# Kernel tuning notes

Hardware: AMD Instinct MI355X
Metric: run time of the kernel (lower is better)

The kernel has to match this reference:

```python
import jax, jax.numpy as jnp
import numpy as np

B, T, I = 64, 512, 512      # batch, timesteps, input feature dim
H1, H2 = 256, 128           # prenet hiddens
C = 1024                    # GRU channels
M = 80                      # mel bins
L = 2                       # residual GRU layers


def setup_inputs() -> dict:
    key = jax.random.key(0)
    ks = jax.random.split(key, 10)
    s = 0.02
    w = lambda k, shape: (jax.random.normal(k, shape, jnp.float32) * s)
    return {
        "inputs": jax.random.normal(ks[0], (B, T, I), jnp.float32),
        # prenet: Linear(M->H1) + ReLU, Linear(H1->H2) + ReLU (dropout off / eval)
        "pre_w0": w(ks[1], (H1, M)), "pre_b0": jnp.zeros((H1,), jnp.float32),
        "pre_w1": w(ks[2], (H2, H1)), "pre_b1": jnp.zeros((H2,), jnp.float32),
        # attention GRU: input I+H2 -> C (PyTorch gate layout [r|z|n])
        "attn_w_ih": w(ks[3], (3 * C, I + H2)), "attn_w_hh": w(ks[4], (3 * C, C)),
        "attn_b_ih": jnp.zeros((3 * C,), jnp.float32), "attn_b_hh": jnp.zeros((3 * C,), jnp.float32),
        # L residual GRUs: C -> C, stacked on leading axis
        "gru_w_ih": w(ks[5], (L, 3 * C, C)), "gru_w_hh": w(ks[6], (L, 3 * C, C)),
        "gru_b_ih": jnp.zeros((L, 3 * C), jnp.float32), "gru_b_hh": jnp.zeros((L, 3 * C), jnp.float32),
        # projection C -> M
        "proj_w": w(ks[7], (M, C)), "proj_b": jnp.zeros((M,), jnp.float32),
    }


def gru_cell(x, h, w_ih, w_hh, b_ih, b_hh):
    # PyTorch GRUCell math, gates ordered [r, z, n]
    gi = x @ w_ih.T + b_ih
    gh = h @ w_hh.T + b_hh
    i_r, i_z, i_n = jnp.split(gi, 3, axis=-1)
    h_r, h_z, h_n = jnp.split(gh, 3, axis=-1)
    r = jax.nn.sigmoid(i_r + h_r)
    z = jax.nn.sigmoid(i_z + h_z)
    n = jnp.tanh(i_n + r * h_n)
    return (1.0 - z) * n + z * h


def reference(inputs, pre_w0, pre_b0, pre_w1, pre_b1,
              attn_w_ih, attn_w_hh, attn_b_ih, attn_b_hh,
              gru_w_ih, gru_w_hh, gru_b_ih, gru_b_hh,
              proj_w, proj_b):
    bsz = inputs.shape[0]
    chan = attn_w_hh.shape[1]
    nlayers = gru_w_ih.shape[0]
    mel = proj_w.shape[0]

    def step(carry, feat):  # feat: [B, I]
        frame, attnh, hidd = carry  # [B,M], [B,C], [L,B,C]
        # prenet on previous frame (dropout disabled, eval-mode reference)
        p = jax.nn.relu(jax.nn.relu(frame @ pre_w0.T + pre_b0) @ pre_w1.T + pre_b1)
        attnh = gru_cell(jnp.concatenate([feat, p], axis=-1), attnh,
                         attn_w_ih, attn_w_hh, attn_b_ih, attn_b_hh)
        x = attnh
        new_hidd = []
        for l in range(nlayers):  # small fixed layer count
            h = gru_cell(x, hidd[l], gru_w_ih[l], gru_w_hh[l], gru_b_ih[l], gru_b_hh[l])
            x = x + h
            new_hidd.append(h)
        frame = x @ proj_w.T + proj_b
        return (frame, attnh, jnp.stack(new_hidd)), frame

    init = (jnp.zeros((bsz, mel), inputs.dtype),
            jnp.zeros((bsz, chan), inputs.dtype),
            jnp.zeros((nlayers, bsz, chan), inputs.dtype))
    _, frames = jax.lax.scan(step, init, jnp.swapaxes(inputs, 0, 1))  # [T,B,M]
    return jnp.swapaxes(frames, 0, 1)  # [B,T,M]
```

## Files before the change

### kernel.cpp

```cpp
#include <hip/hip_runtime.h>
#include <cstddef>


namespace {

constexpr int kB = 64, kT = 512, kI = 512, kH1 = 256, kH2 = 128, kC = 1024, kM = 80;

typedef __attribute__((ext_vector_type(8))) __bf16 bf16x8;
typedef __attribute__((ext_vector_type(4))) float f32x4;

__device__ __forceinline__ float sigm(float x) { return 1.0f / (1.0f + __expf(-x)); }
__device__ __forceinline__ float tanh_(float x) {
  float a = fabsf(x);
  float e = __expf(-2.0f * a);
  float r = (1.0f - e) / (1.0f + e);
  return copysignf(r, x);
}
__device__ __forceinline__ unsigned short f2bf(float x) {
  unsigned u = __builtin_bit_cast(unsigned, x);
  u += 0x7fffu + ((u >> 16) & 1u);
  return (unsigned short)(u >> 16);
}
__device__ __forceinline__ bf16x8 asbf(uint4 v) { return __builtin_bit_cast(bf16x8, v); }
__device__ __forceinline__ f32x4 mfma16(bf16x8 a, bf16x8 b, f32x4 c) {
  return __builtin_amdgcn_mfma_f32_16x16x32_bf16(a, b, c, 0, 0, 0);
}

__global__ __launch_bounds__(256) void k_build_frags(
    const float* __restrict__ srcA, int ldA,
    const float* __restrict__ srcB, int ldB,
    int row0, int K1, int nks, int nrt, unsigned short* __restrict__ dst) {
  int idx = blockIdx.x * 256 + threadIdx.x;
  int lane = idx & 63;
  int ks = (idx >> 6) % nks;
  int rt = idx / (64 * nks);
  if (rt >= nrt) return;
  int row = row0 + rt * 16 + (lane & 15);
  int kk = ks * 32 + ((lane >> 4) & 3) * 8;
  const float* s = (kk < K1) ? (srcA + (size_t)row * ldA + kk)
                             : (srcB + (size_t)row * ldB + (kk - K1));
  unsigned short* d = dst + ((size_t)(rt * nks + ks) * 64 + lane) * 8;
#pragma unroll
  for (int j = 0; j < 8; ++j) d[j] = f2bf(s[j]);
}

__global__ __launch_bounds__(256) void k_transpose(const float* __restrict__ src,
    int R, int Ccols, float* __restrict__ dst) {
  int i = blockIdx.x * 256 + threadIdx.x;
  if (i >= R * Ccols) return;
  int r = i / Ccols, c = i % Ccols;
  dst[c * R + r] = src[r * Ccols + c];
}

__global__ __launch_bounds__(256) void k_prenet(
    const float* __restrict__ inputs, int t,
    const float* __restrict__ pproj,
    const float* __restrict__ proj_b,
    const float* __restrict__ w0t, const float* __restrict__ b0,
    const float* __restrict__ w1t, const float* __restrict__ b1,
    unsigned short* __restrict__ xcat0_cur,
    float* __restrict__ out_frames) {
  int b = blockIdx.x, tid = threadIdx.x;
  __shared__ float sfr[kM];
  __shared__ float sh[kH1];
  __shared__ float sred[160];
  const float* feat = inputs + ((size_t)b * kT + t) * kI;
  unsigned short* dst = xcat0_cur + (size_t)b * 1664;
  float2 f2v = *(const float2*)(feat + tid * 2);
  dst[tid * 2] = f2bf(f2v.x);
  dst[tid * 2 + 1] = f2bf(f2v.y);
  if (t > 0) {
    if (tid < 160) {
      int m = tid >> 1, half = tid & 1;
      const float* pp = pproj + ((size_t)(half * 32) * kM + m) * kB + b;
      float s = 0.0f;
#pragma unroll 8
      for (int r = 0; r < 32; ++r) s += pp[(size_t)r * kM * kB];
      sred[tid] = s;
    }
    __syncthreads();
    if (tid < kM) {
      float f = proj_b[tid] + sred[tid * 2] + sred[tid * 2 + 1];
      sfr[tid] = f;
      out_frames[(size_t)b * kT * kM + (size_t)(t - 1) * kM + tid] = f;
    }
  } else {
    if (tid < kM) sfr[tid] = 0.0f;
  }
  __syncthreads();
  float acc = b0[tid];
#pragma unroll 8
  for (int m = 0; m < kM; ++m) acc = fmaf(w0t[m * kH1 + tid], sfr[m], acc);
  sh[tid] = fmaxf(acc, 0.0f);
  __syncthreads();
  if (tid < kH2) {
    float a = b1[tid];
#pragma unroll 8
    for (int k = 0; k < kH1; ++k) a = fmaf(w1t[k * kH2 + tid], sh[k], a);
    dst[512 + tid] = f2bf(fmaxf(a, 0.0f));
  }
}

template<int NKS, int NB, int BROW>
__global__ __launch_bounds__(512) void k_gru(
    const unsigned short* __restrict__ Ar, const unsigned short* __restrict__ Az,
    const unsigned short* __restrict__ An,
    const unsigned short* __restrict__ Bsrc,
    const float* __restrict__ h_old,
    const float* __restrict__ bih, const float* __restrict__ bhh,
    const float* __restrict__ xin_f32,
    float* __restrict__ h_new_f32,
    unsigned short* __restrict__ h_bf16, int hStride, int hOff,
    unsigned short* __restrict__ x_bf16, int xStride,
    float* __restrict__ xout_f32,
    const float* __restrict__ pw, float* __restrict__ pproj) {
  __shared__ float red[8 * 4 * 64 * 4];
  __shared__ float sx[16 * 16];
  int tid = threadIdx.x;
  int lane = tid & 63, w = tid >> 6, quad = lane >> 4;
  int xcd = blockIdx.x & 7, slot = blockIdx.x >> 3;
  int rt = xcd * 8 + (slot >> 2);
  int bt = slot & 3;
  int b = bt * 16 + (lane & 15);
  int s = (w * NKS) >> 3, e = ((w + 1) * NKS) >> 3;
  const uint4* Bq = (const uint4*)Bsrc + (size_t)b * BROW + quad;
  const uint4* Arq = (const uint4*)Ar + (size_t)rt * NKS * 64 + lane;
  const uint4* Azq = (const uint4*)Az + (size_t)rt * NKS * 64 + lane;
  const uint4* Anq = (const uint4*)An + (size_t)rt * NKS * 64 + lane;
  f32x4 aR = {0.f, 0.f, 0.f, 0.f}, aZ = aR, aNI = aR, aNH = aR;
  for (int ks = s; ks < e; ++ks) {
    bf16x8 bv = asbf(Bq[ks * 4]);
    aR = mfma16(asbf(Arq[ks * 64]), bv, aR);
    aZ = mfma16(asbf(Azq[ks * 64]), bv, aZ);
    if (ks < NB) aNI = mfma16(asbf(Anq[ks * 64]), bv, aNI);
    else         aNH = mfma16(asbf(Anq[ks * 64]), bv, aNH);
  }
  *(f32x4*)(red + ((w * 4 + 0) * 64 + lane) * 4) = aR;
  *(f32x4*)(red + ((w * 4 + 1) * 64 + lane) * 4) = aZ;
  *(f32x4*)(red + ((w * 4 + 2) * 64 + lane) * 4) = aNI;
  *(f32x4*)(red + ((w * 4 + 3) * 64 + lane) * 4) = aNH;
  __syncthreads();
  if (w < 4) {
    int q = lane >> 4, bb = lane & 15;
    float R = 0.f, Z = 0.f, NI = 0.f, NH = 0.f;
#pragma unroll
    for (int ww = 0; ww < 8; ++ww) {
      int base = (ww * 4 * 64 + w * 16 + bb) * 4 + q;
      R  += red[base];
      Z  += red[base + 64 * 4];
      NI += red[base + 2 * 64 * 4];
      NH += red[base + 3 * 64 * 4];
    }
    int c = rt * 16 + w * 4 + q;
    float r = sigm(R + bih[c] + bhh[c]);
    float z = sigm(Z + bih[kC + c] + bhh[kC + c]);
    float n = tanh_(NI + bih[2 * kC + c] + r * (NH + bhh[2 * kC + c]));
    float hold = h_old[c * kB + b];
    float hn = (1.0f - z) * n + z * hold;
    h_new_f32[c * kB + b] = hn;
    h_bf16[(size_t)b * hStride + hOff + c] = f2bf(hn);
    float xo = xin_f32 ? (xin_f32[c * kB + b] + hn) : hn;
    if (x_bf16) x_bf16[(size_t)b * xStride + c] = f2bf(xo);
    if (xout_f32) xout_f32[c * kB + b] = xo;
    if (pw) sx[(w * 4 + q) * 16 + bb] = xo;
  }
  if (pw) {
    __syncthreads();
    for (int idx = tid; idx < kM * 16; idx += 512) {
      int m = idx >> 4, bb = idx & 15;
      const float* wrow = pw + (size_t)m * kC + rt * 16;
      float a = 0.f;
#pragma unroll
      for (int c16 = 0; c16 < 16; ++c16) a += wrow[c16] * sx[c16 * 16 + bb];
      pproj[((size_t)rt * kM + m) * kB + bt * 16 + bb] = a;
    }
  }
}

__global__ __launch_bounds__(256) void k_finalize(const float* __restrict__ pproj,
    const float* __restrict__ proj_b, float* __restrict__ out) {
  int idx = blockIdx.x * 256 + threadIdx.x;
  if (idx >= kB * kM) return;
  int b = idx / kM, m = idx % kM;
  float s = proj_b[m];
#pragma unroll 8
  for (int rt = 0; rt < 64; ++rt) s += pproj[((size_t)rt * kM + m) * kB + b];
  out[(size_t)b * kT * kM + (size_t)(kT - 1) * kM + m] = s;
}

}

extern "C" void kernel_launch(void* const* d_in, const int* in_sizes, int n_in,
                              void* d_out, int out_size, void* d_ws, size_t ws_size,
                              hipStream_t stream) {
  const float* inputs   = (const float*)d_in[0];
  const float* pre_w0   = (const float*)d_in[1];
  const float* pre_b0   = (const float*)d_in[2];
  const float* pre_w1   = (const float*)d_in[3];
  const float* pre_b1   = (const float*)d_in[4];
  const float* attn_wih = (const float*)d_in[5];
  const float* attn_whh = (const float*)d_in[6];
  const float* attn_bih = (const float*)d_in[7];
  const float* attn_bhh = (const float*)d_in[8];
  const float* gru_wih  = (const float*)d_in[9];
  const float* gru_whh  = (const float*)d_in[10];
  const float* gru_bih  = (const float*)d_in[11];
  const float* gru_bhh  = (const float*)d_in[12];
  const float* proj_w   = (const float*)d_in[13];
  const float* proj_b   = (const float*)d_in[14];
  float* out = (float*)d_out;
  char* ws = (char*)d_ws;

  const size_t ATTN_MAT = (size_t)64 * 52 * 64 * 8 * 2;
  const size_t RES_MAT  = (size_t)64 * 64 * 64 * 8 * 2;
  size_t off = 0;
  unsigned short* Aattn[3];
  for (int g = 0; g < 3; ++g) { Aattn[g] = (unsigned short*)(ws + off); off += ATTN_MAT; }
  unsigned short* Ares[2][3];
  for (int l = 0; l < 2; ++l)
    for (int g = 0; g < 3; ++g) { Ares[l][g] = (unsigned short*)(ws + off); off += RES_MAT; }
  float* w0t = (float*)(ws + off); off += (size_t)kM * kH1 * 4;
  float* w1t = (float*)(ws + off); off += (size_t)kH1 * kH2 * 4;
  float* pproj = (float*)(ws + off); off += (size_t)64 * kM * kB * 4;
  size_t zeroBase = off;
  unsigned short* xcat0 = (unsigned short*)(ws + off); off += 2 * (size_t)kB * 1664 * 2;
  unsigned short* xcat1 = (unsigned short*)(ws + off); off += 2 * (size_t)kB * 2048 * 2;
  unsigned short* xcat2 = (unsigned short*)(ws + off); off += 2 * (size_t)kB * 2048 * 2;
  const size_t HB = (size_t)kC * kB;
  float* hA = (float*)(ws + off); off += 2 * HB * 4;
  float* h1 = (float*)(ws + off); off += 2 * HB * 4;
  float* h2 = (float*)(ws + off); off += 2 * HB * 4;
  float* x1 = (float*)(ws + off); off += HB * 4;
  if (off > ws_size) return;

  for (int g = 0; g < 3; ++g)
    k_build_frags<<<16 * 52, 256, 0, stream>>>(attn_wih, 640, attn_whh, kC,
                                               g * kC, 640, 52, 64, Aattn[g]);
  for (int l = 0; l < 2; ++l) {
    const float* wih = gru_wih + (size_t)l * 3 * kC * kC;
    const float* whh = gru_whh + (size_t)l * 3 * kC * kC;
    for (int g = 0; g < 3; ++g)
      k_build_frags<<<16 * 64, 256, 0, stream>>>(wih, kC, whh, kC,
                                                 g * kC, kC, 64, 64, Ares[l][g]);
  }
  k_transpose<<<(kH1 * kM + 255) / 256, 256, 0, stream>>>(pre_w0, kH1, kM, w0t);
  k_transpose<<<(kH2 * kH1 + 255) / 256, 256, 0, stream>>>(pre_w1, kH2, kH1, w1t);
  hipMemsetAsync(ws + zeroBase, 0, off - zeroBase, stream);

  const size_t X0 = (size_t)kB * 1664;
  const size_t XC = (size_t)kB * 2048;
  const float* g_bih1 = gru_bih + 3 * kC;
  const float* g_bhh1 = gru_bhh + 3 * kC;

  for (int t = 0; t < kT; ++t) {
    int cur = t & 1, nxt = cur ^ 1;
    k_prenet<<<kB, 256, 0, stream>>>(inputs, t, pproj, proj_b,
                                     w0t, pre_b0, w1t, pre_b1,
                                     xcat0 + cur * X0, out);
    k_gru<52, 20, 208><<<256, 512, 0, stream>>>(Aattn[0], Aattn[1], Aattn[2],
        xcat0 + cur * X0, hA + cur * HB, attn_bih, attn_bhh,
        nullptr, hA + nxt * HB,
        xcat0 + nxt * X0, 1664, 640,
        xcat1 + cur * XC, 2048,
        nullptr, nullptr, nullptr);
    k_gru<64, 32, 256><<<256, 512, 0, stream>>>(Ares[0][0], Ares[0][1], Ares[0][2],
        xcat1 + cur * XC, h1 + cur * HB, gru_bih, gru_bhh,
        hA + nxt * HB, h1 + nxt * HB,
        xcat1 + nxt * XC, 2048, 1024,
        xcat2 + cur * XC, 2048,
        x1, nullptr, nullptr);
    k_gru<64, 32, 256><<<256, 512, 0, stream>>>(Ares[1][0], Ares[1][1], Ares[1][2],
        xcat2 + cur * XC, h2 + cur * HB, g_bih1, g_bhh1,
        x1, h2 + nxt * HB,
        xcat2 + nxt * XC, 2048, 1024,
        nullptr, 0,
        nullptr, proj_w, pproj);
  }
  k_finalize<<<(kB * kM + 255) / 256, 256, 0, stream>>>(pproj, proj_b, out);
}
```

Before: 22.22 ms.

## Fuse per-timestep kernels into one persistent kernel with grid barriers

Replaces the 4 kernel launches per timestep (prenet plus three GRU layers, 2048 launches in total) with a single persistent 256-block kernel. Phases within a step are separated by a software grid barrier built on atomics. Cross-block data is read and written through relaxed agent-scope atomics so that values stay coherent across blocks without a kernel boundary. This removes launch and inter-kernel gap overhead, but it relies on all 256 blocks being co-resident, and the atomic 8-byte B-fragment loads may cost some memory efficiency.

```diff
diff --git a/kernel.cpp b/kernel.cpp
--- a/kernel.cpp
+++ b/kernel.cpp
@@ -24,6 +24,22 @@
 __device__ __forceinline__ bf16x8 asbf(uint4 v) { return __builtin_bit_cast(bf16x8, v); }
 __device__ __forceinline__ f32x4 mfma16(bf16x8 a, bf16x8 b, f32x4 c) {
   return __builtin_amdgcn_mfma_f32_16x16x32_bf16(a, b, c, 0, 0, 0);
+}
+
+__device__ __forceinline__ float ld_f(const float* p) {
+  return __hip_atomic_load(p, __ATOMIC_RELAXED, __HIP_MEMORY_SCOPE_AGENT);
+}
+__device__ __forceinline__ void st_f(float* p, float v) {
+  __hip_atomic_store(p, v, __ATOMIC_RELAXED, __HIP_MEMORY_SCOPE_AGENT);
+}
+__device__ __forceinline__ unsigned long long ld_u64(const unsigned long long* p) {
+  return __hip_atomic_load(p, __ATOMIC_RELAXED, __HIP_MEMORY_SCOPE_AGENT);
+}
+__device__ __forceinline__ void st_u32(unsigned* p, unsigned v) {
+  __hip_atomic_store(p, v, __ATOMIC_RELAXED, __HIP_MEMORY_SCOPE_AGENT);
+}
+__device__ __forceinline__ void st_u16(unsigned short* p, unsigned short v) {
+  __hip_atomic_store(p, v, __ATOMIC_RELAXED, __HIP_MEMORY_SCOPE_AGENT);
 }
 
 __global__ __launch_bounds__(256) void k_build_frags(
@@ -52,88 +68,106 @@
   dst[c * R + r] = src[r * Ccols + c];
 }
 
-__global__ __launch_bounds__(256) void k_prenet(
-    const float* __restrict__ inputs, int t,
-    const float* __restrict__ pproj,
-    const float* __restrict__ proj_b,
-    const float* __restrict__ w0t, const float* __restrict__ b0,
-    const float* __restrict__ w1t, const float* __restrict__ b1,
-    unsigned short* __restrict__ xcat0_cur,
-    float* __restrict__ out_frames) {
-  int b = blockIdx.x, tid = threadIdx.x;
-  __shared__ float sfr[kM];
-  __shared__ float sh[kH1];
-  __shared__ float sred[160];
-  const float* feat = inputs + ((size_t)b * kT + t) * kI;
-  unsigned short* dst = xcat0_cur + (size_t)b * 1664;
-  float2 f2v = *(const float2*)(feat + tid * 2);
-  dst[tid * 2] = f2bf(f2v.x);
-  dst[tid * 2 + 1] = f2bf(f2v.y);
+struct P {
+  const float* inputs;
+  const float* w0t; const float* pre_b0;
+  const float* w1t; const float* pre_b1;
+  const unsigned short* Aa0; const unsigned short* Aa1; const unsigned short* Aa2;
+  const float* attn_bih; const float* attn_bhh;
+  const unsigned short* A10; const unsigned short* A11; const unsigned short* A12;
+  const unsigned short* A20; const unsigned short* A21; const unsigned short* A22;
+  const float* gru_bih; const float* gru_bhh;
+  const float* proj_w; const float* proj_b;
+  unsigned short* xcat0; unsigned short* xcat1; unsigned short* xcat2;
+  float* hA; float* h1; float* h2; float* x1; float* pproj;
+  float* out;
+  unsigned* bar_cnt; unsigned* bar_gen;
+};
+
+__device__ __forceinline__ void gridbar(unsigned* cnt, unsigned* gen, unsigned& g) {
+  __syncthreads();
+  if (threadIdx.x == 0) {
+    unsigned a = __hip_atomic_fetch_add(cnt, 1u, __ATOMIC_RELEASE, __HIP_MEMORY_SCOPE_AGENT);
+    if (a == 255u) {
+      __hip_atomic_store(cnt, 0u, __ATOMIC_RELAXED, __HIP_MEMORY_SCOPE_AGENT);
+      __hip_atomic_store(gen, g + 1u, __ATOMIC_RELEASE, __HIP_MEMORY_SCOPE_AGENT);
+    } else {
+      while (__hip_atomic_load(gen, __ATOMIC_RELAXED, __HIP_MEMORY_SCOPE_AGENT) == g) {}
+    }
+  }
+  __syncthreads();
+  g += 1u;
+}
+
+__device__ __forceinline__ void prenet_phase(const P& p, int b, int t,
+    unsigned short* xc0cur, float* sfr, float* sh, float* sred) {
+  int tid = threadIdx.x;
+  unsigned short* dst = xc0cur + (size_t)b * 1664;
+  if (tid < 256) {
+    const float* feat = p.inputs + ((size_t)b * kT + t) * kI;
+    float2 f2v = *(const float2*)(feat + tid * 2);
+    unsigned pack = (unsigned)f2bf(f2v.x) | ((unsigned)f2bf(f2v.y) << 16);
+    st_u32((unsigned*)dst + tid, pack);
+  }
   if (t > 0) {
     if (tid < 160) {
       int m = tid >> 1, half = tid & 1;
-      const float* pp = pproj + ((size_t)(half * 32) * kM + m) * kB + b;
+      const float* pp = p.pproj + ((size_t)(half * 32) * kM + m) * kB + b;
       float s = 0.0f;
 #pragma unroll 8
-      for (int r = 0; r < 32; ++r) s += pp[(size_t)r * kM * kB];
+      for (int r = 0; r < 32; ++r) s += ld_f(pp + (size_t)r * kM * kB);
       sred[tid] = s;
     }
     __syncthreads();
     if (tid < kM) {
-      float f = proj_b[tid] + sred[tid * 2] + sred[tid * 2 + 1];
+      float f = p.proj_b[tid] + sred[tid * 2] + sred[tid * 2 + 1];
       sfr[tid] = f;
-      out_frames[(size_t)b * kT * kM + (size_t)(t - 1) * kM + tid] = f;
+      p.out[(size_t)b * kT * kM + (size_t)(t - 1) * kM + tid] = f;
     }
   } else {
     if (tid < kM) sfr[tid] = 0.0f;
   }
   __syncthreads();
-  float acc = b0[tid];
+  if (tid < 256) {
+    float acc = p.pre_b0[tid];
 #pragma unroll 8
-  for (int m = 0; m < kM; ++m) acc = fmaf(w0t[m * kH1 + tid], sfr[m], acc);
-  sh[tid] = fmaxf(acc, 0.0f);
+    for (int m = 0; m < kM; ++m) acc = fmaf(p.w0t[m * kH1 + tid], sfr[m], acc);
+    sh[tid] = fmaxf(acc, 0.0f);
+  }
   __syncthreads();
   if (tid < kH2) {
-    float a = b1[tid];
+    float a = p.pre_b1[tid];
 #pragma unroll 8
-    for (int k = 0; k < kH1; ++k) a = fmaf(w1t[k * kH2 + tid], sh[k], a);
-    dst[512 + tid] = f2bf(fmaxf(a, 0.0f));
+    for (int k = 0; k < kH1; ++k) a = fmaf(p.w1t[k * kH2 + tid], sh[k], a);
+    st_u16(dst + 512 + tid, f2bf(fmaxf(a, 0.0f)));
   }
 }
 
 template<int NKS, int NB, int BROW>
-__global__ __launch_bounds__(512) void k_gru(
-    const unsigned short* __restrict__ Ar, const unsigned short* __restrict__ Az,
-    const unsigned short* __restrict__ An,
-    const unsigned short* __restrict__ Bsrc,
-    const float* __restrict__ h_old,
-    const float* __restrict__ bih, const float* __restrict__ bhh,
-    const float* __restrict__ xin_f32,
-    float* __restrict__ h_new_f32,
-    unsigned short* __restrict__ h_bf16, int hStride, int hOff,
-    unsigned short* __restrict__ x_bf16, int xStride,
-    float* __restrict__ xout_f32,
-    const float* __restrict__ pw, float* __restrict__ pproj) {
-  __shared__ float red[8 * 4 * 64 * 4];
-  __shared__ float sx[16 * 16];
-  int tid = threadIdx.x;
-  int lane = tid & 63, w = tid >> 6, quad = lane >> 4;
-  int xcd = blockIdx.x & 7, slot = blockIdx.x >> 3;
-  int rt = xcd * 8 + (slot >> 2);
-  int bt = slot & 3;
+__device__ __forceinline__ void gru_phase(int rt, int bt,
+    const unsigned short* Ar, const unsigned short* Az, const unsigned short* An,
+    const unsigned short* Bsrc, const float* h_old,
+    const float* bih, const float* bhh, const float* xin_f32,
+    float* h_new_f32, unsigned short* h_bf16, int hStride, int hOff,
+    unsigned short* x_bf16, int xStride, float* xout_f32,
+    const float* pw, float* pproj, float* red, float* sx) {
+  int tid = threadIdx.x, lane = tid & 63, w = tid >> 6, quad = lane >> 4;
   int b = bt * 16 + (lane & 15);
   int s = (w * NKS) >> 3, e = ((w + 1) * NKS) >> 3;
-  const uint4* Bq = (const uint4*)Bsrc + (size_t)b * BROW + quad;
+  const unsigned long long* B8 =
+      (const unsigned long long*)Bsrc + ((size_t)b * BROW + quad) * 2;
   const uint4* Arq = (const uint4*)Ar + (size_t)rt * NKS * 64 + lane;
   const uint4* Azq = (const uint4*)Az + (size_t)rt * NKS * 64 + lane;
   const uint4* Anq = (const uint4*)An + (size_t)rt * NKS * 64 + lane;
   f32x4 aR = {0.f, 0.f, 0.f, 0.f}, aZ = aR, aNI = aR, aNH = aR;
   for (int ks = s; ks < e; ++ks) {
-    bf16x8 bv = asbf(Bq[ks * 4]);
-    aR = mfma16(asbf(Arq[ks * 64]), bv, aR);
-    aZ = mfma16(asbf(Azq[ks * 64]), bv, aZ);
-    if (ks < NB) aNI = mfma16(asbf(Anq[ks * 64]), bv, aNI);
-    else         aNH = mfma16(asbf(Anq[ks * 64]), bv, aNH);
+    union { unsigned long long q[2]; bf16x8 v; } u;
+    u.q[0] = ld_u64(B8 + (size_t)ks * 8);
+    u.q[1] = ld_u64(B8 + (size_t)ks * 8 + 1);
+    aR = mfma16(asbf(Arq[ks * 64]), u.v, aR);
+    aZ = mfma16(asbf(Azq[ks * 64]), u.v, aZ);
+    if (ks < NB) aNI = mfma16(asbf(Anq[ks * 64]), u.v, aNI);
+    else         aNH = mfma16(asbf(Anq[ks * 64]), u.v, aNH);
   }
   *(f32x4*)(red + ((w * 4 + 0) * 64 + lane) * 4) = aR;
   *(f32x4*)(red + ((w * 4 + 1) * 64 + lane) * 4) = aZ;
@@ -142,6 +176,7 @@
   __syncthreads();
   if (w < 4) {
     int q = lane >> 4, bb = lane & 15;
+    int b2 = bt * 16 + bb;
     float R = 0.f, Z = 0.f, NI = 0.f, NH = 0.f;
 #pragma unroll
     for (int ww = 0; ww < 8; ++ww) {
@@ -155,13 +190,13 @@
     float r = sigm(R + bih[c] + bhh[c]);
     float z = sigm(Z + bih[kC + c] + bhh[kC + c]);
     float n = tanh_(NI + bih[2 * kC + c] + r * (NH + bhh[2 * kC + c]));
-    float hold = h_old[c * kB + b];
+    float hold = ld_f(h_old + c * kB + b2);
     float hn = (1.0f - z) * n + z * hold;
-    h_new_f32[c * kB + b] = hn;
-    h_bf16[(size_t)b * hStride + hOff + c] = f2bf(hn);
-    float xo = xin_f32 ? (xin_f32[c * kB + b] + hn) : hn;
-    if (x_bf16) x_bf16[(size_t)b * xStride + c] = f2bf(xo);
-    if (xout_f32) xout_f32[c * kB + b] = xo;
+    st_f(h_new_f32 + c * kB + b2, hn);
+    st_u16(h_bf16 + (size_t)b2 * hStride + hOff + c, f2bf(hn));
+    float xo = xin_f32 ? (ld_f(xin_f32 + c * kB + b2) + hn) : hn;
+    if (x_bf16) st_u16(x_bf16 + (size_t)b2 * xStride + c, f2bf(xo));
+    if (xout_f32) st_f(xout_f32 + c * kB + b2, xo);
     if (pw) sx[(w * 4 + q) * 16 + bb] = xo;
   }
   if (pw) {
@@ -172,20 +207,55 @@
       float a = 0.f;
 #pragma unroll
       for (int c16 = 0; c16 < 16; ++c16) a += wrow[c16] * sx[c16 * 16 + bb];
-      pproj[((size_t)rt * kM + m) * kB + bt * 16 + bb] = a;
-    }
-  }
-}
-
-__global__ __launch_bounds__(256) void k_finalize(const float* __restrict__ pproj,
-    const float* __restrict__ proj_b, float* __restrict__ out) {
-  int idx = blockIdx.x * 256 + threadIdx.x;
-  if (idx >= kB * kM) return;
-  int b = idx / kM, m = idx % kM;
-  float s = proj_b[m];
+      st_f(pproj + ((size_t)rt * kM + m) * kB + bt * 16 + bb, a);
+    }
+  }
+}
+
+__global__ __launch_bounds__(512, 2) void k_decoder(P p) {
+  __shared__ float red[8192];
+  __shared__ float sx[256];
+  int xcd = blockIdx.x & 7, slot = blockIdx.x >> 3;
+  int rt = xcd * 8 + (slot >> 2);
+  int bt = slot & 3;
+  unsigned g = 0;
+  const size_t X0 = (size_t)kB * 1664;
+  const size_t XC = (size_t)kB * 2048;
+  const size_t HB = (size_t)kC * kB;
+  const float* g_bih1 = p.gru_bih + 3 * kC;
+  const float* g_bhh1 = p.gru_bhh + 3 * kC;
+
+  for (int t = 0; t < kT; ++t) {
+    int cur = t & 1, nxt = cur ^ 1;
+    if (bt == 0)
+      prenet_phase(p, rt, t, p.xcat0 + cur * X0, red, red + 128, red + 512);
+    gridbar(p.bar_cnt, p.bar_gen, g);
+    gru_phase<52, 20, 208>(rt, bt, p.Aa0, p.Aa1, p.Aa2,
+        p.xcat0 + cur * X0, p.hA + cur * HB, p.attn_bih, p.attn_bhh, nullptr,
+        p.hA + nxt * HB, p.xcat0 + nxt * X0, 1664, 640,
+        p.xcat1 + cur * XC, 2048, nullptr, nullptr, nullptr, red, sx);
+    gridbar(p.bar_cnt, p.bar_gen, g);
+    gru_phase<64, 32, 256>(rt, bt, p.A10, p.A11, p.A12,
+        p.xcat1 + cur * XC, p.h1 + cur * HB, p.gru_bih, p.gru_bhh,
+        p.hA + nxt * HB,
+        p.h1 + nxt * HB, p.xcat1 + nxt * XC, 2048, 1024,
+        p.xcat2 + cur * XC, 2048, p.x1, nullptr, nullptr, red, sx);
+    gridbar(p.bar_cnt, p.bar_gen, g);
+    gru_phase<64, 32, 256>(rt, bt, p.A20, p.A21, p.A22,
+        p.xcat2 + cur * XC, p.h2 + cur * HB, g_bih1, g_bhh1,
+        p.x1,
+        p.h2 + nxt * HB, p.xcat2 + nxt * XC, 2048, 1024,
+        nullptr, 0, nullptr, p.proj_w, p.pproj, red, sx);
+    gridbar(p.bar_cnt, p.bar_gen, g);
+  }
+  if (bt == 0 && threadIdx.x < kM) {
+    int m = threadIdx.x;
+    float s = p.proj_b[m];
 #pragma unroll 8
-  for (int rt = 0; rt < 64; ++rt) s += pproj[((size_t)rt * kM + m) * kB + b];
-  out[(size_t)b * kT * kM + (size_t)(kT - 1) * kM + m] = s;
+    for (int r = 0; r < 64; ++r)
+      s += ld_f(p.pproj + ((size_t)r * kM + m) * kB + rt);
+    p.out[((size_t)rt * kT + (kT - 1)) * kM + m] = s;
+  }
 }
 
 }
@@ -223,6 +293,8 @@
   float* w1t = (float*)(ws + off); off += (size_t)kH1 * kH2 * 4;
   float* pproj = (float*)(ws + off); off += (size_t)64 * kM * kB * 4;
   size_t zeroBase = off;
+  unsigned* bar_cnt = (unsigned*)(ws + off); off += 128;
+  unsigned* bar_gen = (unsigned*)(ws + off); off += 128;
   unsigned short* xcat0 = (unsigned short*)(ws + off); off += 2 * (size_t)kB * 1664 * 2;
   unsigned short* xcat1 = (unsigned short*)(ws + off); off += 2 * (size_t)kB * 2048 * 2;
   unsigned short* xcat2 = (unsigned short*)(ws + off); off += 2 * (size_t)kB * 2048 * 2;
@@ -247,34 +319,19 @@
   k_transpose<<<(kH2 * kH1 + 255) / 256, 256, 0, stream>>>(pre_w1, kH2, kH1, w1t);
   hipMemsetAsync(ws + zeroBase, 0, off - zeroBase, stream);
 
-  const size_t X0 = (size_t)kB * 1664;
-  const size_t XC = (size_t)kB * 2048;
-  const float* g_bih1 = gru_bih + 3 * kC;
-  const float* g_bhh1 = gru_bhh + 3 * kC;
-
-  for (int t = 0; t < kT; ++t) {
-    int cur = t & 1, nxt = cur ^ 1;
-    k_prenet<<<kB, 256, 0, stream>>>(inputs, t, pproj, proj_b,
-                                     w0t, pre_b0, w1t, pre_b1,
-                                     xcat0 + cur * X0, out);
-    k_gru<52, 20, 208><<<256, 512, 0, stream>>>(Aattn[0], Aattn[1], Aattn[2],
-        xcat0 + cur * X0, hA + cur * HB, attn_bih, attn_bhh,
-        nullptr, hA + nxt * HB,
-        xcat0 + nxt * X0, 1664, 640,
-        xcat1 + cur * XC, 2048,
-        nullptr, nullptr, nullptr);
-    k_gru<64, 32, 256><<<256, 512, 0, stream>>>(Ares[0][0], Ares[0][1], Ares[0][2],
-        xcat1 + cur * XC, h1 + cur * HB, gru_bih, gru_bhh,
-        hA + nxt * HB, h1 + nxt * HB,
-        xcat1 + nxt * XC, 2048, 1024,
-        xcat2 + cur * XC, 2048,
-        x1, nullptr, nullptr);
-    k_gru<64, 32, 256><<<256, 512, 0, stream>>>(Ares[1][0], Ares[1][1], Ares[1][2],
-        xcat2 + cur * XC, h2 + cur * HB, g_bih1, g_bhh1,
-        x1, h2 + nxt * HB,
-        xcat2 + nxt * XC, 2048, 1024,
-        nullptr, 0,
-        nullptr, proj_w, pproj);
-  }
-  k_finalize<<<(kB * kM + 255) / 256, 256, 0, stream>>>(pproj, proj_b, out);
-}
+  P p;
+  p.inputs = inputs;
+  p.w0t = w0t; p.pre_b0 = pre_b0; p.w1t = w1t; p.pre_b1 = pre_b1;
+  p.Aa0 = Aattn[0]; p.Aa1 = Aattn[1]; p.Aa2 = Aattn[2];
+  p.attn_bih = attn_bih; p.attn_bhh = attn_bhh;
+  p.A10 = Ares[0][0]; p.A11 = Ares[0][1]; p.A12 = Ares[0][2];
+  p.A20 = Ares[1][0]; p.A21 = Ares[1][1]; p.A22 = Ares[1][2];
+  p.gru_bih = gru_bih; p.gru_bhh = gru_bhh;
+  p.proj_w = proj_w; p.proj_b = proj_b;
+  p.xcat0 = xcat0; p.xcat1 = xcat1; p.xcat2 = xcat2;
+  p.hA = hA; p.h1 = h1; p.h2 = h2; p.x1 = x1; p.pproj = pproj;
+  p.out = out;
+  p.bar_cnt = bar_cnt; p.bar_gen = bar_gen;
+
+  k_decoder<<<256, 512, 0, stream>>>(p);
+}
```

Result: slower. 31.41 ms (+41.4%).
